# Kernel optimization log

Hardware: AMD Instinct MI355X
Metric: run time of the kernel (lower is better)

## Reference

```python
import jax, jax.numpy as jnp
import numpy as np


def _lga_pass(x, filters, radius):
    # x: [N, C, H, W]; filters: [N, (2r+1)^2, H, W]
    # out[n,c,h,w] = sum_{i,j in [-r,r]} filters[n,(i+r)*(2r+1)+(j+r),h,w] * x[n,c,h+i,w+j]
    N, C, H, W = x.shape
    k = 2 * radius + 1
    xp = jnp.pad(x, ((0, 0), (0, 0), (radius, radius), (radius, radius)))
    out = jnp.zeros_like(x)
    idx = 0
    for i in range(k):  # fixed small kernel loop (25 taps), accumulates without materializing [N,C,H,W,25]
        for j in range(k):
            out = out + filters[:, idx:idx + 1] * xp[:, :, i:i + H, j:j + W]
            idx += 1
    return out


def setup_inputs() -> dict:
    key = jax.random.key(0)
    k1, k2 = jax.random.split(key)
    input1 = jax.random.normal(k1, (2, 64, 256, 512), dtype=jnp.float32)
    input2 = jax.random.uniform(k2, (2, 25, 256, 512), dtype=jnp.float32)
    return {"input1": input1, "input2": input2, "radius": 2}


def reference(input1, input2, radius):
    # LGA applied twice with the same per-pixel filters (Lga2Function.forward)
    temp = _lga_pass(input1, input2, radius)
    out = _lga_pass(temp, input2, radius)
    return out
```

## Files before the change

### kernel.cpp

```cpp
#include <hip/hip_runtime.h>
#include <hip/hip_fp16.h>


typedef __fp16 h2v __attribute__((ext_vector_type(2)));

#define OH 12
#define OW 60
#define USH 40

__device__ __forceinline__ unsigned pkh(float a, float b) {
    union { h2v h; unsigned u; } c;
    c.h = __builtin_amdgcn_cvt_pkrtz(a, b);
    return c.u;
}

#define M(ac, fv, xv, sf, sx) \
    asm("v_fma_mix_f32 %0, %1, %2, %0 op_sel:[" #sf "," #sx ",0] op_sel_hi:[1,1,0]" \
        : "+v"(ac) : "v"(fv), "v"(xv));

#define ROWM(T, w0, w1, w2, w3) \
  M(a0,frA[T+0],w0,0,0) M(a1,frA[T+0],w0,1,1) M(a2,frB[T+0],w1,0,0) M(a3,frB[T+0],w1,1,1) \
  M(a0,frA[T+1],w0,0,1) M(a1,frA[T+1],w1,1,0) M(a2,frB[T+1],w1,0,1) M(a3,frB[T+1],w2,1,0) \
  M(a0,frA[T+2],w1,0,0) M(a1,frA[T+2],w1,1,1) M(a2,frB[T+2],w2,0,0) M(a3,frB[T+2],w2,1,1) \
  M(a0,frA[T+3],w1,0,1) M(a1,frA[T+3],w2,1,0) M(a2,frB[T+3],w2,0,1) M(a3,frB[T+3],w3,1,0) \
  M(a0,frA[T+4],w2,0,0) M(a1,frA[T+4],w2,1,1) M(a2,frB[T+4],w3,0,0) M(a3,frB[T+4],w3,1,1)

#define PASS(BUF, ROWBASE) { \
    a0 = 0.f; a1 = 0.f; a2 = 0.f; a3 = 0.f; \
    _Pragma("unroll") \
    for (int i = 0; i < 5; ++i) { \
        const int b = ((ROWBASE) + i) * USH + 2 * s; \
        uint2 lo = *(const uint2*)&(BUF)[b]; \
        uint2 hi = *(const uint2*)&(BUF)[b + 2]; \
        ROWM(5 * i, lo.x, lo.y, hi.x, hi.y) \
    } }

#define LBAR() { asm volatile("s_waitcnt lgkmcnt(0)" ::: "memory"); \
                 __builtin_amdgcn_s_barrier(); asm volatile("" ::: "memory"); }

#define BODY(CC, SXR, SXL, STB, NXI0, NXI1, NXL0, NXL1) { \
    if ((CC) + 2 < CPB) { \
        if (ok0) NXI0 = *(const float4*)pfp0; \
        if (ok1) NXI1 = *(const float4*)pfp1; \
    } \
    pfp0 += HW; pfp1 += HW; \
    float a0, a1, a2, a3; \
    PASS(SXR, r) \
    (STB)[r * USH + 1 + 2 * s] = pkh(a0, a1); \
    (STB)[r * USH + 2 + 2 * s] = pkh(a2, a3); \
    if ((CC) + 1 < CPB) { \
        *(uint2*)&(SXL)[l0u] = make_uint2(pkh(NXL0.x, NXL0.y), pkh(NXL0.z, NXL0.w)); \
        if (has1) *(uint2*)&(SXL)[l1u] = make_uint2(pkh(NXL1.x, NXL1.y), pkh(NXL1.z, NXL1.w)); \
    } \
    LBAR(); \
    PASS(STB, rc - 2) \
    if (prow) { \
        if (s >= 1 && gwb + 1 < W)  *(float2*)op       = make_float2(a0, a1); \
        if (s <= 14 && gwb + 3 < W) *(float2*)(op + 2) = make_float2(a2, a3); \
    } \
    op += HW; \
}

__global__ __launch_bounds__(256)
void lga2_fused(const float* __restrict__ x, const float* __restrict__ f,
                float* __restrict__ out, int N, int C, int H, int W, int CPB) {
    const int tid = threadIdx.x;
    const int r = tid >> 4;
    const int s = tid & 15;
    const int oh0 = blockIdx.y * OH;
    const int ow0 = blockIdx.x * OW;
    const int CG = C / CPB;
    const int n  = blockIdx.z / CG;
    const int c0 = (blockIdx.z % CG) * CPB;
    const int HW = H * W;

    __shared__ unsigned sx0[20 * USH], sx1[20 * USH];
    __shared__ unsigned st0[16 * USH], st1[16 * USH];

    if (tid < 64) {
        unsigned* stz = (tid < 32) ? st0 : st1;
        int i = tid & 31, row = i & 15;
        stz[row * USH + ((i & 16) ? 33 : 0)] = 0u;
    }

    const int gh_f = oh0 - 2 + r;
    const int gwb  = ow0 - 2 + 4 * s;
    const bool rowok = (gh_f >= 0) && (gh_f < H);
    const bool p0ok = rowok && (gwb >= 0) && (gwb + 1 < W);
    const bool p1ok = rowok && (gwb + 3 < W);
    const float* fb = f + (size_t)(n * 25) * HW + (size_t)(rowok ? gh_f : 0) * W;

    unsigned frA[25], frB[25];
    #pragma unroll
    for (int t = 0; t < 25; ++t) {
        float2 v01 = p0ok ? *(const float2*)(fb + (size_t)t * HW + gwb)
                          : make_float2(0.f, 0.f);
        float2 v23 = p1ok ? *(const float2*)(fb + (size_t)t * HW + gwb + 2)
                          : make_float2(0.f, 0.f);
        frA[t] = pkh(v01.x, v01.y);
        frB[t] = pkh(v23.x, v23.y);
        if ((t % 5) == 4) __builtin_amdgcn_sched_barrier(0);
    }
    #pragma unroll
    for (int t = 0; t < 25; ++t)
        asm volatile("" : "+v"(frA[t]), "+v"(frB[t]));

    const int i1 = tid + 256;
    const bool has1 = (tid < 340 - 256);
    const int row0 = tid / 17, v0 = tid - row0 * 17;
    const int row1 = i1 / 17,  v1 = i1 - row1 * 17;
    const int g0h = oh0 - 4 + row0, g0c = ow0 - 4 + 4 * v0;
    const int g1h = oh0 - 4 + row1, g1c = ow0 - 4 + 4 * v1;
    const bool ok0 = (g0h >= 0) && (g0h < H) && (g0c >= 0) && (g0c + 3 < W);
    const bool ok1 = has1 && (g1h >= 0) && (g1h < H) && (g1c >= 0) && (g1c + 3 < W);
    const int off0 = ok0 ? (g0h * W + g0c) : 0;
    const int off1 = ok1 ? (g1h * W + g1c) : 0;
    const int l0u = row0 * USH + 2 * v0;
    const int l1u = row1 * USH + 2 * v1;

    const float4 z4 = make_float4(0.f, 0.f, 0.f, 0.f);
    const float* xc = x + (size_t)(n * C + c0) * HW;

    {
        float4 p = ok0 ? *(const float4*)(xc + off0) : z4;
        *(uint2*)&sx0[l0u] = make_uint2(pkh(p.x, p.y), pkh(p.z, p.w));
        if (has1) {
            float4 q = ok1 ? *(const float4*)(xc + off1) : z4;
            *(uint2*)&sx0[l1u] = make_uint2(pkh(q.x, q.y), pkh(q.z, q.w));
        }
    }
    float4 nxA0 = z4, nxA1 = z4, nxB0 = z4, nxB1 = z4;
    if (CPB > 1) {
        if (ok0) nxB0 = *(const float4*)(xc + HW + off0);
        if (ok1) nxB1 = *(const float4*)(xc + HW + off1);
    }
    const float* pfp0 = xc + 2 * (size_t)HW + off0;
    const float* pfp1 = xc + 2 * (size_t)HW + off1;
    __syncthreads();

    const bool prow = (r >= 2) && (r <= 13) && (gh_f < H);
    const int rc = (r < 2) ? 2 : ((r > 13) ? 13 : r);
    float* op = out + ((size_t)(n * C + c0) * H + gh_f) * W + gwb;

    for (int cc = 0; cc < CPB; cc += 2) {
        BODY(cc,     sx0, sx1, st0, nxA0, nxA1, nxB0, nxB1)
        BODY(cc + 1, sx1, sx0, st1, nxB0, nxB1, nxA0, nxA1)
    }
}

extern "C" void kernel_launch(void* const* d_in, const int* in_sizes, int n_in,
                              void* d_out, int out_size, void* d_ws, size_t ws_size,
                              hipStream_t stream) {
    const float* x = (const float*)d_in[0];
    const float* f = (const float*)d_in[1];
    float* out = (float*)d_out;

    const int N = 2, C = 64, H = 256, W = 512;
    const int CPB = 16;
    const int CG = C / CPB;

    dim3 grid((W + OW - 1) / OW,
              (H + OH - 1) / OH,
              N * CG);
    lga2_fused<<<grid, 256, 0, stream>>>(x, f, out, N, C, H, W, CPB);
}
```

Before: 84.12 us.

## Switch tap accumulation to packed fp16 FMA with split even/odd accumulators

Replaces the scalar v_fma_mix_f32 accumulation (four fp32 accumulators) with v_pk_fma_f16 on packed half2 pairs. Shifted pixel pairs are built with shifts and ORs, and even and odd filter rows go to separate accumulators that are summed at the end. This halves the FMA instruction count per tap. In exchange, accumulation happens in fp16 over 25 taps per pass and two passes, which lowers accuracy. The change also doubles channels per block to 32, pins waves_per_eu to 3, and moves a scheduling barrier.

```diff
diff --git a/kernel.cpp b/kernel.cpp
--- a/kernel.cpp
+++ b/kernel.cpp
@@ -14,26 +14,32 @@
     return c.u;
 }
 
-#define M(ac, fv, xv, sf, sx) \
-    asm("v_fma_mix_f32 %0, %1, %2, %0 op_sel:[" #sf "," #sx ",0] op_sel_hi:[1,1,0]" \
-        : "+v"(ac) : "v"(fv), "v"(xv));
+#define PKF(ac, fv, xv) \
+    asm("v_pk_fma_f16 %0, %1, %2, %0" : "+v"(ac) : "v"(fv), "v"(xv));
 
-#define ROWM(T, w0, w1, w2, w3) \
-  M(a0,frA[T+0],w0,0,0) M(a1,frA[T+0],w0,1,1) M(a2,frB[T+0],w1,0,0) M(a3,frB[T+0],w1,1,1) \
-  M(a0,frA[T+1],w0,0,1) M(a1,frA[T+1],w1,1,0) M(a2,frB[T+1],w1,0,1) M(a3,frB[T+1],w2,1,0) \
-  M(a0,frA[T+2],w1,0,0) M(a1,frA[T+2],w1,1,1) M(a2,frB[T+2],w2,0,0) M(a3,frB[T+2],w2,1,1) \
-  M(a0,frA[T+3],w1,0,1) M(a1,frA[T+3],w2,1,0) M(a2,frB[T+3],w2,0,1) M(a3,frB[T+3],w3,1,0) \
-  M(a0,frA[T+4],w2,0,0) M(a1,frA[T+4],w2,1,1) M(a2,frB[T+4],w3,0,0) M(a3,frB[T+4],w3,1,1)
+#define ROWP(i, w0, w1, w2, w3, D01, D23) { \
+    const unsigned A01 = ((w0) >> 16) | ((w1) << 16); \
+    const unsigned A12 = ((w1) >> 16) | ((w2) << 16); \
+    const unsigned A23 = ((w2) >> 16) | ((w3) << 16); \
+    PKF(D01, frA[5*(i)+0], w0)  PKF(D01, frA[5*(i)+1], A01) \
+    PKF(D01, frA[5*(i)+2], w1)  PKF(D01, frA[5*(i)+3], A12) \
+    PKF(D01, frA[5*(i)+4], w2) \
+    PKF(D23, frB[5*(i)+0], w1)  PKF(D23, frB[5*(i)+1], A12) \
+    PKF(D23, frB[5*(i)+2], w2)  PKF(D23, frB[5*(i)+3], A23) \
+    PKF(D23, frB[5*(i)+4], w3) }
 
-#define PASS(BUF, ROWBASE) { \
-    a0 = 0.f; a1 = 0.f; a2 = 0.f; a3 = 0.f; \
+#define PASSP(BUF, ROWBASE) { \
+    unsigned e01 = 0u, o01 = 0u, e23 = 0u, o23 = 0u; \
     _Pragma("unroll") \
     for (int i = 0; i < 5; ++i) { \
         const int b = ((ROWBASE) + i) * USH + 2 * s; \
         uint2 lo = *(const uint2*)&(BUF)[b]; \
         uint2 hi = *(const uint2*)&(BUF)[b + 2]; \
-        ROWM(5 * i, lo.x, lo.y, hi.x, hi.y) \
-    } }
+        if (i & 1) { ROWP(i, lo.x, lo.y, hi.x, hi.y, o01, o23) } \
+        else       { ROWP(i, lo.x, lo.y, hi.x, hi.y, e01, e23) } \
+    } \
+    asm("v_pk_add_f16 %0, %1, %2" : "=v"(s01) : "v"(e01), "v"(o01)); \
+    asm("v_pk_add_f16 %0, %1, %2" : "=v"(s23) : "v"(e23), "v"(o23)); }
 
 #define LBAR() { asm volatile("s_waitcnt lgkmcnt(0)" ::: "memory"); \
                  __builtin_amdgcn_s_barrier(); asm volatile("" ::: "memory"); }
@@ -44,24 +50,29 @@
         if (ok1) NXI1 = *(const float4*)pfp1; \
     } \
     pfp0 += HW; pfp1 += HW; \
-    float a0, a1, a2, a3; \
-    PASS(SXR, r) \
-    (STB)[r * USH + 1 + 2 * s] = pkh(a0, a1); \
-    (STB)[r * USH + 2 + 2 * s] = pkh(a2, a3); \
+    unsigned s01, s23; \
+    PASSP(SXR, r) \
+    (STB)[r * USH + 1 + 2 * s] = s01; \
+    (STB)[r * USH + 2 + 2 * s] = s23; \
     if ((CC) + 1 < CPB) { \
         *(uint2*)&(SXL)[l0u] = make_uint2(pkh(NXL0.x, NXL0.y), pkh(NXL0.z, NXL0.w)); \
         if (has1) *(uint2*)&(SXL)[l1u] = make_uint2(pkh(NXL1.x, NXL1.y), pkh(NXL1.z, NXL1.w)); \
     } \
     LBAR(); \
-    PASS(STB, rc - 2) \
+    PASSP(STB, rc - 2) \
     if (prow) { \
-        if (s >= 1 && gwb + 1 < W)  *(float2*)op       = make_float2(a0, a1); \
-        if (s <= 14 && gwb + 3 < W) *(float2*)(op + 2) = make_float2(a2, a3); \
+        union { unsigned u; h2v h; } U01, U23; \
+        U01.u = s01; U23.u = s23; \
+        if (s >= 1 && gwb + 1 < W) \
+            *(float2*)op = make_float2((float)U01.h.x, (float)U01.h.y); \
+        if (s <= 14 && gwb + 3 < W) \
+            *(float2*)(op + 2) = make_float2((float)U23.h.x, (float)U23.h.y); \
     } \
     op += HW; \
 }
 
 __global__ __launch_bounds__(256)
+__attribute__((amdgpu_waves_per_eu(3, 3)))
 void lga2_fused(const float* __restrict__ x, const float* __restrict__ f,
                 float* __restrict__ out, int N, int C, int H, int W, int CPB) {
     const int tid = threadIdx.x;
@@ -99,7 +110,7 @@
                           : make_float2(0.f, 0.f);
         frA[t] = pkh(v01.x, v01.y);
         frB[t] = pkh(v23.x, v23.y);
-        if ((t % 5) == 4) __builtin_amdgcn_sched_barrier(0);
+        if (t == 12) __builtin_amdgcn_sched_barrier(0);
     }
     #pragma unroll
     for (int t = 0; t < 25; ++t)
@@ -156,7 +167,7 @@
     float* out = (float*)d_out;
 
     const int N = 2, C = 64, H = 256, W = 512;
-    const int CPB = 16;
+    const int CPB = 32;
     const int CG = C / CPB;
 
     dim3 grid((W + OW - 1) / OW,
```

After: 92.91 us. +10.4%, slower.
